# Kernel optimization log

Measured on AMD Instinct MI355X. Metric: run time of the kernel, lower is better.

## Reference

```python
import jax, jax.numpy as jnp
import numpy as np

D_MODEL = 2048
N_HEADS = 16
HEAD_DIM = D_MODEL // N_HEADS  # 128
B, T = 2, 2048


def setup_inputs() -> dict:
    key = jax.random.key(0)
    ks = jax.random.split(key, 9)
    s = 0.02
    x = jax.random.normal(ks[0], (B, T, D_MODEL), dtype=jnp.float32)
    # Per-head projection weights (stacked over heads); torch Linear y = x @ W^T + b,
    # here W is stored as [H, d_model, head_dim] so y = einsum('btc,hcd->bhtd').
    Wq = jax.random.normal(ks[1], (N_HEADS, D_MODEL, HEAD_DIM), dtype=jnp.float32) * s
    bq = jax.random.normal(ks[2], (N_HEADS, HEAD_DIM), dtype=jnp.float32) * s
    Wk = jax.random.normal(ks[3], (N_HEADS, D_MODEL, HEAD_DIM), dtype=jnp.float32) * s
    bk = jax.random.normal(ks[4], (N_HEADS, HEAD_DIM), dtype=jnp.float32) * s
    Wv = jax.random.normal(ks[5], (N_HEADS, D_MODEL, HEAD_DIM), dtype=jnp.float32) * s
    bv = jax.random.normal(ks[6], (N_HEADS, HEAD_DIM), dtype=jnp.float32) * s
    Wo = jax.random.normal(ks[7], (D_MODEL, D_MODEL), dtype=jnp.float32) * s  # used as y @ Wo
    bo = jax.random.normal(ks[8], (D_MODEL,), dtype=jnp.float32) * s
    return {"x": x, "Wq": Wq, "bq": bq, "Wk": Wk, "bk": bk,
            "Wv": Wv, "bv": bv, "Wo": Wo, "bo": bo}


def reference(x, Wq, bq, Wk, bk, Wv, bv, Wo, bo):
    # x: [B, T, C]; per-head Q/K/V projections -> [B, H, T, D]
    Bn, Tn, C = x.shape
    H, _, D = Wq.shape
    scale = D ** (-0.5)
    q = jnp.einsum('btc,hcd->bhtd', x, Wq) + bq[None, :, None, :]
    k = jnp.einsum('btc,hcd->bhtd', x, Wk) + bk[None, :, None, :]
    v = jnp.einsum('btc,hcd->bhtd', x, Wv) + bv[None, :, None, :]
    # scores [B, H, T, T] with additive causal mask (finfo.min above the diagonal)
    scores = jnp.einsum('bhtd,bhsd->bhts', q, k) * scale
    neg = jnp.finfo(scores.dtype).min
    causal = jnp.triu(jnp.full((Tn, Tn), neg, dtype=scores.dtype), k=1)
    probs = jax.nn.softmax(scores + causal, axis=-1)
    y = jnp.einsum('bhts,bhsd->bhtd', probs, v)  # [B, H, T, D]
    # concat heads along feature dim (head order preserved) then output projection
    y = y.transpose(0, 2, 1, 3).reshape(Bn, Tn, H * D)
    return y @ Wo + bo
```

## Files before the change

kernel.cpp:

```cpp
#include <hip/hip_runtime.h>
#include <stdint.h>

typedef unsigned short u16;
typedef __attribute__((ext_vector_type(4))) u16 u16x4;
typedef __attribute__((ext_vector_type(8))) u16 u16x8;
typedef __attribute__((ext_vector_type(8))) __bf16 bf16x8;
typedef __attribute__((ext_vector_type(4))) float f32x4;
typedef __attribute__((ext_vector_type(16))) float f32x16;

#define D_MODEL 2048
#define N_HEADS 16
#define HEAD_DIM 128
#define BATCH 2
#define SEQ 2048
#define M_TOT (BATCH*SEQ)
#define N_QKV (3*D_MODEL)

__device__ __forceinline__ u16 f2b(float f) {
  union { float f; uint32_t u; } c; c.f = f;
  uint32_t u = c.u;
  uint32_t r = (u + 0x7fffu + ((u >> 16) & 1u)) >> 16;
  return (u16)r;
}

__device__ __forceinline__ void gl_lds16(const u16* g, u16* l) {
  __builtin_amdgcn_global_load_lds(
      (const __attribute__((address_space(1))) uint32_t*)g,
      (__attribute__((address_space(3))) uint32_t*)l, 16, 0, 0);
}

template <int N> __device__ __forceinline__ void waitvm() {
  if constexpr (N == 6)      asm volatile("s_waitcnt vmcnt(6)" ::: "memory");
  else if constexpr (N == 5) asm volatile("s_waitcnt vmcnt(5)" ::: "memory");
  else                       asm volatile("s_waitcnt vmcnt(0)" ::: "memory");
}


__global__ void cast_x_kernel(const float* __restrict__ x, u16* __restrict__ xb, int n) {
  int i = (blockIdx.x * blockDim.x + threadIdx.x) * 4;
  if (i >= n) return;
  f32x4 v = *(const f32x4*)(x + i);
  u16x4 o;
  o[0] = f2b(v[0]); o[1] = f2b(v[1]); o[2] = f2b(v[2]); o[3] = f2b(v[3]);
  *(u16x4*)(xb + i) = o;
}

__global__ void trans_wqkv_kernel(const float* __restrict__ Wq, const float* __restrict__ Wk,
                                  const float* __restrict__ Wv, u16* __restrict__ Wt) {
  __shared__ u16 Tl[128][72];
  const int hh = blockIdx.y;
  const int qkv = hh >> 4, h = hh & 15;
  const float* src = (qkv == 0 ? Wq : qkv == 1 ? Wk : Wv) + (size_t)h * 2048 * 128;
  const int k0 = blockIdx.x * 64;
  const int tid = threadIdx.x;
  for (int it = 0; it < 32; ++it) {
    int idx = it * 256 + tid;
    int k = idx >> 7, d = idx & 127;
    Tl[d][k] = f2b(src[(size_t)(k0 + k) * 128 + d]);
  }
  __syncthreads();
  for (int it = 0; it < 32; ++it) {
    int idx = it * 256 + tid;
    int d = idx >> 6, kk = idx & 63;
    Wt[(size_t)(hh * 128 + d) * 2048 + k0 + kk] = Tl[d][kk];
  }
}

__global__ void trans_wo_kernel(const float* __restrict__ Wo, u16* __restrict__ Wot) {
  __shared__ u16 Tl[128][72];
  const int k0 = blockIdx.x * 64;
  const int n0 = blockIdx.y * 128;
  const int tid = threadIdx.x;
  for (int it = 0; it < 32; ++it) {
    int idx = it * 256 + tid;
    int k = idx >> 7, n = idx & 127;
    Tl[n][k] = f2b(Wo[(size_t)(k0 + k) * 2048 + n0 + n]);
  }
  __syncthreads();
  for (int it = 0; it < 32; ++it) {
    int idx = it * 256 + tid;
    int d = idx >> 6, kk = idx & 63;
    Wot[(size_t)(n0 + d) * 2048 + k0 + kk] = Tl[d][kk];
  }
}

__global__ void transpose_v_kernel(const u16* __restrict__ vb, u16* __restrict__ vt) {
  __shared__ u16 Tl[128 * 65];
  const int bh = blockIdx.y;
  const int t0 = blockIdx.x * 64;
  const int tid = threadIdx.x;
  const u16* src = vb + (size_t)bh * 2048 * 128;
  u16* dstp = vt + (size_t)bh * 128 * 2048;
#pragma unroll
  for (int c = 0; c < 4; ++c) {
    int ci = c * 256 + tid;
    int tr = ci >> 4, d0 = (ci & 15) * 8;
    u16x8 v = *(const u16x8*)(src + (size_t)(t0 + tr) * 128 + d0);
#pragma unroll
    for (int e = 0; e < 8; ++e) Tl[(d0 + e) * 65 + tr] = v[e];
  }
  __syncthreads();
#pragma unroll
  for (int it = 0; it < 32; ++it) {
    int idx = it * 256 + tid;
    int d = idx >> 6, tt = idx & 63;
    dstp[(size_t)d * 2048 + t0 + ((tt & 15) * 4 + (tt >> 4))] = Tl[d * 65 + tt];
  }
}

__global__ __launch_bounds__(512, 2) void gemm_qkv_kernel(
    const u16* __restrict__ A, const u16* __restrict__ B,
    u16* __restrict__ qo, u16* __restrict__ ko, u16* __restrict__ vo,
    const float* __restrict__ bq, const float* __restrict__ bk, const float* __restrict__ bv) {
  __shared__ u16 LS[3][20480];
  const int bid0 = blockIdx.x;
  const int gid = (bid0 & 7) * 32 + (bid0 >> 3);
  const int G = gid >> 4, l = gid & 15;
  const int m0 = ((G & 3) * 4 + (l & 3)) * 256;
  const int n0 = ((G >> 2) * 4 + (l >> 2)) * 384;

  const int tid = threadIdx.x, lane = tid & 63, w = tid >> 6;
  const int wm = (w >> 2) * 128, wn = (w & 3) * 96;
  const int l31 = lane & 31, g2 = lane >> 5;

  int aoff[2], boff[3];
#pragma unroll
  for (int l2 = 0; l2 < 2; ++l2) {
    int ci = l2 * 512 + tid, t = ci >> 3, x = (ci & 7) ^ (t & 7);
    aoff[l2] = (m0 + 2 * t + (x >> 2)) * 2048 + (x & 3) * 8;
  }
#pragma unroll
  for (int l2 = 0; l2 < 3; ++l2) {
    int ci = l2 * 512 + tid, t = ci >> 3, x = (ci & 7) ^ (t & 7);
    boff[l2] = (n0 + 2 * t + (x >> 2)) * 2048 + (x & 3) * 8;
  }
  const int adl = tid * 8;
  const int bdl = 8192 + tid * 8;

  f32x16 acc[4][3];
#pragma unroll
  for (int ai = 0; ai < 4; ++ai)
#pragma unroll
    for (int bj = 0; bj < 3; ++bj)
#pragma unroll
      for (int e = 0; e < 16; ++e) acc[ai][bj][e] = 0.f;

#pragma unroll
  for (int t = 0; t < 2; ++t) {
#pragma unroll
    for (int l2 = 0; l2 < 2; ++l2) gl_lds16(A + aoff[l2] + t * 32, LS[t] + adl + l2 * 4096);
#pragma unroll
    for (int l2 = 0; l2 < 3; ++l2) gl_lds16(B + boff[l2] + t * 32, LS[t] + bdl + l2 * 4096);
  }
  waitvm<5>();
  __builtin_amdgcn_s_barrier();

  int s = 0;
  for (int kt = 0; kt < 64; ++kt) {
    if (kt < 62) {
      const int s2 = (s == 0) ? 2 : s - 1;
      const int k2 = (kt + 2) * 32;
#pragma unroll
      for (int l2 = 0; l2 < 2; ++l2) gl_lds16(A + aoff[l2] + k2, LS[s2] + adl + l2 * 4096);
#pragma unroll
      for (int l2 = 0; l2 < 3; ++l2) gl_lds16(B + boff[l2] + k2, LS[s2] + bdl + l2 * 4096);
    }
    const char* base = (const char*)LS[s];
#pragma unroll
    for (int kk = 0; kk < 2; ++kk) {
      bf16x8 af[4];
#pragma unroll
      for (int ai = 0; ai < 4; ++ai) {
        int r = wm + ai * 32 + l31;
        int x = ((r & 1) << 2) | (2 * kk + g2);
        af[ai] = *(const bf16x8*)(base + (r >> 1) * 128 + 16 * (x ^ ((r >> 1) & 7)));
      }
      __builtin_amdgcn_s_setprio(1);
#pragma unroll
      for (int bj = 0; bj < 3; ++bj) {
        int rb = wn + bj * 32 + l31;
        int xb2 = ((rb & 1) << 2) | (2 * kk + g2);
        bf16x8 bfr = *(const bf16x8*)(base + 16384 + (rb >> 1) * 128 + 16 * (xb2 ^ ((rb >> 1) & 7)));
#pragma unroll
        for (int ai = 0; ai < 4; ++ai)
          acc[ai][bj] = __builtin_amdgcn_mfma_f32_32x32x16_bf16(af[ai], bfr, acc[ai][bj], 0, 0, 0);
      }
      __builtin_amdgcn_s_setprio(0);
    }
    if (kt < 62)       waitvm<5>();
    else if (kt == 62) waitvm<0>();
    __builtin_amdgcn_s_barrier();
    s = (s == 2) ? 0 : s + 1;
  }

  const float qscale = 0.08838834764831845f * 1.4426950408889634f;
#pragma unroll
  for (int bj = 0; bj < 3; ++bj) {
    const int n = n0 + wn + bj * 32 + l31;
    const int qkv = n >> 11, hh = (n >> 7) & 15, d = n & 127;
    const float* bias = (qkv == 0) ? bq : (qkv == 1) ? bk : bv;
    u16* dst = (qkv == 0) ? qo : (qkv == 1) ? ko : vo;
    const float bv_ = bias[n & 2047];
#pragma unroll
    for (int ai = 0; ai < 4; ++ai)
#pragma unroll
      for (int e = 0; e < 16; ++e) {
        int row = (e & 3) + 8 * (e >> 2) + 4 * g2;
        int gm = m0 + wm + ai * 32 + row;
        float val = acc[ai][bj][e] + bv_;
        if (qkv == 0) val *= qscale;
        int b = gm >> 11, t = gm & 2047;
        dst[((size_t)(b * 16 + hh) * 2048 + t) * 128 + d] = f2b(val);
      }
  }
}

__global__ __launch_bounds__(512, 2) void gemm_out_kernel(
    const u16* __restrict__ A, const u16* __restrict__ B,
    float* __restrict__ outf, const float* __restrict__ bo) {
  __shared__ u16 LS[3][24576];
  const int bid0 = blockIdx.x;
  const int gid = (bid0 & 7) * 32 + (bid0 >> 3);
  const int G = gid >> 4, l = gid & 15;
  const int m0 = ((G & 3) * 4 + (l & 3)) * 256;
  const int n0 = ((G >> 2) * 4 + (l >> 2)) * 128;

  const int tid = threadIdx.x, lane = tid & 63, w = tid >> 6;
  const int wm = (w >> 1) * 64, wn = (w & 1) * 64;
  const int lr = lane & 15, g = lane >> 4;
  const int kx = (lr & 7) << 4;

  int aoff[4], boff[2];
#pragma unroll
  for (int l2 = 0; l2 < 4; ++l2) {
    int ci = l2 * 512 + tid, r = ci >> 3, gj = ci & 7;
    aoff[l2] = (m0 + r) * 2048 + (gj ^ (r & 7)) * 8;
  }
#pragma unroll
  for (int l2 = 0; l2 < 2; ++l2) {
    int ci = l2 * 512 + tid, r = ci >> 3, gj = ci & 7;
    boff[l2] = (n0 + r) * 2048 + (gj ^ (r & 7)) * 8;
  }
  const int adl = tid * 8;
  const int bdl = 16384 + tid * 8;

  f32x4 acc[4][4];
  const f32x4 zero = {0.f, 0.f, 0.f, 0.f};
#pragma unroll
  for (int ai = 0; ai < 4; ++ai)
#pragma unroll
    for (int bj = 0; bj < 4; ++bj) acc[ai][bj] = zero;

#pragma unroll
  for (int t = 0; t < 2; ++t) {
#pragma unroll
    for (int l2 = 0; l2 < 4; ++l2) gl_lds16(A + aoff[l2] + t * 64, LS[t] + adl + l2 * 4096);
#pragma unroll
    for (int l2 = 0; l2 < 2; ++l2) gl_lds16(B + boff[l2] + t * 64, LS[t] + bdl + l2 * 4096);
  }
  waitvm<6>();
  __builtin_amdgcn_s_barrier();

  int s = 0;
  for (int kt = 0; kt < 32; ++kt) {
    if (kt < 30) {
      const int s2 = (s == 0) ? 2 : s - 1;
      const int k2 = (kt + 2) * 64;
#pragma unroll
      for (int l2 = 0; l2 < 4; ++l2) gl_lds16(A + aoff[l2] + k2, LS[s2] + adl + l2 * 4096);
#pragma unroll
      for (int l2 = 0; l2 < 2; ++l2) gl_lds16(B + boff[l2] + k2, LS[s2] + bdl + l2 * 4096);
    }
    const char* base = (const char*)LS[s];
#pragma unroll
    for (int h = 0; h < 2; ++h) {
      bf16x8 af[4];
#pragma unroll
      for (int ai = 0; ai < 4; ++ai) {
        int r = wm + ai * 16 + lr;
        af[ai] = *(const bf16x8*)(base + r * 128 + ((h * 64 + 16 * g) ^ kx));
      }
      __builtin_amdgcn_s_setprio(1);
#pragma unroll
      for (int bj = 0; bj < 4; ++bj) {
        int rb = wn + bj * 16 + lr;
        bf16x8 bfr = *(const bf16x8*)(base + 32768 + rb * 128 + ((h * 64 + 16 * g) ^ kx));
#pragma unroll
        for (int ai = 0; ai < 4; ++ai)
          acc[ai][bj] = __builtin_amdgcn_mfma_f32_16x16x32_bf16(af[ai], bfr, acc[ai][bj], 0, 0, 0);
      }
      __builtin_amdgcn_s_setprio(0);
    }
    if (kt < 30)       waitvm<6>();
    else if (kt == 30) waitvm<0>();
    __builtin_amdgcn_s_barrier();
    s = (s == 2) ? 0 : s + 1;
  }

  const int rbase = g * 4;
#pragma unroll
  for (int bj = 0; bj < 4; ++bj) {
    const int gn = n0 + wn + bj * 16 + lr;
    const float bv_ = bo[gn];
#pragma unroll
    for (int ai = 0; ai < 4; ++ai)
#pragma unroll
      for (int r = 0; r < 4; ++r) {
        int gm = m0 + wm + ai * 16 + rbase + r;
        outf[(size_t)gm * 2048 + gn] = acc[ai][bj][r] + bv_;
      }
  }
}

__global__ __launch_bounds__(256) void attn_kernel(
    const u16* __restrict__ qg, const u16* __restrict__ kg,
    const u16* __restrict__ vtg, u16* __restrict__ y) {
  __shared__ u16 Kb[2][64 * 128];
  __shared__ u16 Vb[2][128 * 64];
  __shared__ u16 Pl[4][32 * 64];
  const int tid = threadIdx.x, lane = tid & 63, w = tid >> 6;
  const int bid = blockIdx.x;
  const int bh = bid & 31, qt = 15 - (bid >> 5);
  const int b = bh >> 4, h = bh & 15;
  const int lr = lane & 15, lk = (lane >> 4) * 8;
  const u16* Qp = qg + (size_t)bh * (2048 * 128);
  const u16* Kp = kg + (size_t)bh * (2048 * 128);
  const u16* Vp = vtg + (size_t)bh * (128 * 2048);

  int koff[4], voff[4], dstc[4];
#pragma unroll
  for (int c = 0; c < 4; ++c) {
    int ci = c * 256 + tid;
    dstc[c] = ci * 8;
    int kr = ci >> 4, kj = ci & 15;
    koff[c] = kr * 128 + (kj ^ (kr & 7)) * 8;
    int vd = ci >> 3, vj = ci & 7;
    voff[c] = vd * 2048 + (vj ^ (vd & 7)) * 8;
  }
  const int kxor = (lr & 7) << 4;
  const int rbase = (lane >> 4) * 4;
  const f32x4 zero = {0.f, 0.f, 0.f, 0.f};

  const int q0 = qt * 128;
  const int qw = q0 + w * 32;
  const int nt = 2 * qt + 2;

  bf16x8 qf[2][4];
#pragma unroll
  for (int s = 0; s < 2; ++s)
#pragma unroll
    for (int i = 0; i < 4; ++i)
      qf[s][i] = *(const bf16x8*)(Qp + (size_t)(qw + s * 16 + lr) * 128 + i * 32 + lk);

  f32x4 o[2][8];
#pragma unroll
  for (int s = 0; s < 2; ++s)
#pragma unroll
    for (int f = 0; f < 8; ++f) o[s][f] = zero;
  float mrow[2][4], lrow[2][4];
#pragma unroll
  for (int s = 0; s < 2; ++s)
#pragma unroll
    for (int r = 0; r < 4; ++r) { mrow[s][r] = -1e30f; lrow[s][r] = 0.f; }

#pragma unroll
  for (int c = 0; c < 4; ++c) gl_lds16(Kp + koff[c], Kb[0] + dstc[c]);
#pragma unroll
  for (int c = 0; c < 4; ++c) gl_lds16(Vp + voff[c], Vb[0] + dstc[c]);
  __syncthreads();

  int cur = 0;
  for (int t = 0; t < nt; ++t) {
    const int s0 = t * 64;
    if (t + 1 < nt) {
      const size_t skn = (size_t)(s0 + 64) * 128;
#pragma unroll
      for (int c = 0; c < 4; ++c) gl_lds16(Kp + skn + koff[c], Kb[cur ^ 1] + dstc[c]);
#pragma unroll
      for (int c = 0; c < 4; ++c) gl_lds16(Vp + (s0 + 64) + voff[c], Vb[cur ^ 1] + dstc[c]);
    }
    if (s0 <= qw + 31) {
      const char* Kc = (const char*)Kb[cur];
      f32x4 sf[2][4];
      __builtin_amdgcn_s_setprio(1);
#pragma unroll
      for (int sj = 0; sj < 4; ++sj) {
        f32x4 a0 = zero, a1 = zero;
#pragma unroll
        for (int i = 0; i < 4; ++i) {
          bf16x8 kf = *(const bf16x8*)(Kc + ((((sj * 16 + lr) * 256) + (i * 32 + lk) * 2) ^ kxor));
          a0 = __builtin_amdgcn_mfma_f32_16x16x32_bf16(qf[0][i], kf, a0, 0, 0, 0);
          a1 = __builtin_amdgcn_mfma_f32_16x16x32_bf16(qf[1][i], kf, a1, 0, 0, 0);
        }
        sf[0][sj] = a0; sf[1][sj] = a1;
      }
      __builtin_amdgcn_s_setprio(0);

      char* Pc = (char*)Pl[w];
      const bool diag = (s0 + 63 > qw);
      float pmax[2][4];
      bool need = false;
#pragma unroll
      for (int s = 0; s < 2; ++s)
#pragma unroll
        for (int r = 0; r < 4; ++r) {
          if (diag) {
            const int rq = qw + s * 16 + rbase + r;
#pragma unroll
            for (int sj = 0; sj < 4; ++sj)
              if (s0 + sj * 16 + lr > rq) sf[s][sj][r] = -1e30f;
          }
          float pm = fmaxf(fmaxf(sf[s][0][r], sf[s][1][r]),
                           fmaxf(sf[s][2][r], sf[s][3][r]));
          pmax[s][r] = pm;
          need |= (pm > mrow[s][r] + 8.f);
        }
      if (__any(need)) {
#pragma unroll
        for (int s = 0; s < 2; ++s)
#pragma unroll
          for (int r = 0; r < 4; ++r) {
            float pm = pmax[s][r];
            pm = fmaxf(pm, __shfl_xor(pm, 1));
            pm = fmaxf(pm, __shfl_xor(pm, 2));
            pm = fmaxf(pm, __shfl_xor(pm, 4));
            pm = fmaxf(pm, __shfl_xor(pm, 8));
            float mnew = fmaxf(mrow[s][r], pm);
            float sfac = __builtin_amdgcn_exp2f(mrow[s][r] - mnew);
            mrow[s][r] = mnew;
            lrow[s][r] *= sfac;
#pragma unroll
            for (int f = 0; f < 8; ++f) o[s][f][r] *= sfac;
          }
      }
#pragma unroll
      for (int s = 0; s < 2; ++s)
#pragma unroll
        for (int r = 0; r < 4; ++r) {
          const int prow = s * 16 + rbase + r;
          u16x4 pk;
          float ps = 0.f;
#pragma unroll
          for (int sj = 0; sj < 4; ++sj) {
            float p = __builtin_amdgcn_exp2f(sf[s][sj][r] - mrow[s][r]);
            ps += p;
            pk[sj] = f2b(p);
          }
          lrow[s][r] += ps;
          *(u16x4*)(Pc + ((prow * 128 + lr * 8) ^ ((prow & 7) << 4))) = pk;
        }

      const char* Vc = (const char*)Vb[cur];
      __builtin_amdgcn_s_setprio(1);
#pragma unroll
      for (int st = 0; st < 2; ++st) {
        bf16x8 pf0 = *(const bf16x8*)(Pc + (((lr * 128) + (st * 32 + lk) * 2) ^ kxor));
        bf16x8 pf1 = *(const bf16x8*)(Pc + ((((16 + lr) * 128) + (st * 32 + lk) * 2) ^ kxor));
#pragma unroll
        for (int f = 0; f < 8; ++f) {
          bf16x8 vf = *(const bf16x8*)(Vc + ((((f * 16 + lr) * 128) + (st * 32 + lk) * 2) ^ kxor));
          o[0][f] = __builtin_amdgcn_mfma_f32_16x16x32_bf16(pf0, vf, o[0][f], 0, 0, 0);
          o[1][f] = __builtin_amdgcn_mfma_f32_16x16x32_bf16(pf1, vf, o[1][f], 0, 0, 0);
        }
      }
      __builtin_amdgcn_s_setprio(0);
    }
    __syncthreads();
    cur ^= 1;
  }

#pragma unroll
  for (int s = 0; s < 2; ++s)
#pragma unroll
    for (int r = 0; r < 4; ++r) {
      float l = lrow[s][r];
      l += __shfl_xor(l, 1);
      l += __shfl_xor(l, 2);
      l += __shfl_xor(l, 4);
      l += __shfl_xor(l, 8);
      const float rinv = __builtin_amdgcn_rcpf(l);
      const int row = qw + s * 16 + rbase + r;
#pragma unroll
      for (int f = 0; f < 8; ++f)
        y[((size_t)b * 2048 + row) * 2048 + h * 128 + f * 16 + lr] =
            f2b(o[s][f][r] * rinv);
    }
}


extern "C" void kernel_launch(void* const* d_in, const int* in_sizes, int n_in,
                              void* d_out, int out_size, void* d_ws, size_t ws_size,
                              hipStream_t stream) {
  const float* x  = (const float*)d_in[0];
  const float* Wq = (const float*)d_in[1];
  const float* bq = (const float*)d_in[2];
  const float* Wk = (const float*)d_in[3];
  const float* bk = (const float*)d_in[4];
  const float* Wv = (const float*)d_in[5];
  const float* bv = (const float*)d_in[6];
  const float* Wo = (const float*)d_in[7];
  const float* bo = (const float*)d_in[8];
  float* out = (float*)d_out;
  char* ws = (char*)d_ws;

  u16* xb  = (u16*)(ws + 0);
  u16* Wt  = (u16*)(ws + 16777216);
  u16* qb  = (u16*)(ws + 41943040);
  u16* kb  = (u16*)(ws + 58720256);
  u16* vb  = (u16*)(ws + 75497472);
  u16* Wot = Wt;
  u16* vtb = (u16*)(ws + 25165824);
  u16* yb  = xb;

  cast_x_kernel<<<8192, 256, 0, stream>>>(x, xb, M_TOT * D_MODEL);
  trans_wqkv_kernel<<<dim3(32, 48), 256, 0, stream>>>(Wq, Wk, Wv, Wt);
  gemm_qkv_kernel<<<256, 512, 0, stream>>>(xb, Wt, qb, kb, vb, bq, bk, bv);
  trans_wo_kernel<<<dim3(32, 16), 256, 0, stream>>>(Wo, Wot);
  transpose_v_kernel<<<dim3(32, 32), 256, 0, stream>>>(vb, vtb);
  attn_kernel<<<512, 256, 0, stream>>>(qb, kb, vtb, yb);
  gemm_out_kernel<<<256, 512, 0, stream>>>(yb, Wot, out, bo);
}
```

Measured before the change: 282.8 us.

## Fuse prep kernels, write V transposed from QKV GEMM, use packed bf16 convert

Merges the x cast and the QKV weight transpose into one launch. The QKV GEMM epilogue now writes V directly in the permuted transposed layout the attention kernel expects, which removes the separate V transpose kernel and its round trip through memory. The softmax P conversion uses the hardware packed bf16 convert instead of manual rounding. The V epilogue stores are strided along d, so that write pattern may coalesce poorly.

```diff
diff --git a/kernel.cpp b/kernel.cpp
--- a/kernel.cpp
+++ b/kernel.cpp
@@ -35,24 +35,25 @@
   else                       asm volatile("s_waitcnt vmcnt(0)" ::: "memory");
 }
 
-
-__global__ void cast_x_kernel(const float* __restrict__ x, u16* __restrict__ xb, int n) {
-  int i = (blockIdx.x * blockDim.x + threadIdx.x) * 4;
-  if (i >= n) return;
-  f32x4 v = *(const f32x4*)(x + i);
-  u16x4 o;
-  o[0] = f2b(v[0]); o[1] = f2b(v[1]); o[2] = f2b(v[2]); o[3] = f2b(v[3]);
-  *(u16x4*)(xb + i) = o;
-}
-
-__global__ void trans_wqkv_kernel(const float* __restrict__ Wq, const float* __restrict__ Wk,
-                                  const float* __restrict__ Wv, u16* __restrict__ Wt) {
+__global__ __launch_bounds__(256) void prep_kernel(
+    const float* __restrict__ x, u16* __restrict__ xb,
+    const float* __restrict__ Wq, const float* __restrict__ Wk,
+    const float* __restrict__ Wv, u16* __restrict__ Wt) {
   __shared__ u16 Tl[128][72];
-  const int hh = blockIdx.y;
+  const int bid = blockIdx.x, tid = threadIdx.x;
+  if (bid < 8192) {
+    int i = (bid * 256 + tid) * 4;
+    f32x4 v = *(const f32x4*)(x + i);
+    u16x4 o;
+    o[0] = f2b(v[0]); o[1] = f2b(v[1]); o[2] = f2b(v[2]); o[3] = f2b(v[3]);
+    *(u16x4*)(xb + i) = o;
+    return;
+  }
+  const int rel = bid - 8192;
+  const int k0 = (rel & 31) * 64;
+  const int hh = rel >> 5;
   const int qkv = hh >> 4, h = hh & 15;
   const float* src = (qkv == 0 ? Wq : qkv == 1 ? Wk : Wv) + (size_t)h * 2048 * 128;
-  const int k0 = blockIdx.x * 64;
-  const int tid = threadIdx.x;
   for (int it = 0; it < 32; ++it) {
     int idx = it * 256 + tid;
     int k = idx >> 7, d = idx & 127;
@@ -81,30 +82,6 @@
     int idx = it * 256 + tid;
     int d = idx >> 6, kk = idx & 63;
     Wot[(size_t)(n0 + d) * 2048 + k0 + kk] = Tl[d][kk];
-  }
-}
-
-__global__ void transpose_v_kernel(const u16* __restrict__ vb, u16* __restrict__ vt) {
-  __shared__ u16 Tl[128 * 65];
-  const int bh = blockIdx.y;
-  const int t0 = blockIdx.x * 64;
-  const int tid = threadIdx.x;
-  const u16* src = vb + (size_t)bh * 2048 * 128;
-  u16* dstp = vt + (size_t)bh * 128 * 2048;
-#pragma unroll
-  for (int c = 0; c < 4; ++c) {
-    int ci = c * 256 + tid;
-    int tr = ci >> 4, d0 = (ci & 15) * 8;
-    u16x8 v = *(const u16x8*)(src + (size_t)(t0 + tr) * 128 + d0);
-#pragma unroll
-    for (int e = 0; e < 8; ++e) Tl[(d0 + e) * 65 + tr] = v[e];
-  }
-  __syncthreads();
-#pragma unroll
-  for (int it = 0; it < 32; ++it) {
-    int idx = it * 256 + tid;
-    int d = idx >> 6, tt = idx & 63;
-    dstp[(size_t)d * 2048 + t0 + ((tt & 15) * 4 + (tt >> 4))] = Tl[d * 65 + tt];
   }
 }
 
@@ -199,7 +176,7 @@
     const int n = n0 + wn + bj * 32 + l31;
     const int qkv = n >> 11, hh = (n >> 7) & 15, d = n & 127;
     const float* bias = (qkv == 0) ? bq : (qkv == 1) ? bk : bv;
-    u16* dst = (qkv == 0) ? qo : (qkv == 1) ? ko : vo;
+    u16* dst = (qkv == 0) ? qo : ko;
     const float bv_ = bias[n & 2047];
 #pragma unroll
     for (int ai = 0; ai < 4; ++ai)
@@ -210,7 +187,12 @@
         float val = acc[ai][bj][e] + bv_;
         if (qkv == 0) val *= qscale;
         int b = gm >> 11, t = gm & 2047;
-        dst[((size_t)(b * 16 + hh) * 2048 + t) * 128 + d] = f2b(val);
+        if (qkv == 2) {
+          int tt = (t & ~63) | ((t & 15) * 4 + ((t >> 4) & 3));
+          vo[((size_t)(b * 16 + hh)) * 262144 + (size_t)d * 2048 + tt] = f2b(val);
+        } else {
+          dst[((size_t)(b * 16 + hh) * 2048 + t) * 128 + d] = f2b(val);
+        }
       }
   }
 }
@@ -438,16 +420,16 @@
 #pragma unroll
         for (int r = 0; r < 4; ++r) {
           const int prow = s * 16 + rbase + r;
-          u16x4 pk;
-          float ps = 0.f;
-#pragma unroll
-          for (int sj = 0; sj < 4; ++sj) {
-            float p = __builtin_amdgcn_exp2f(sf[s][sj][r] - mrow[s][r]);
-            ps += p;
-            pk[sj] = f2b(p);
-          }
-          lrow[s][r] += ps;
-          *(u16x4*)(Pc + ((prow * 128 + lr * 8) ^ ((prow & 7) << 4))) = pk;
+          float p0 = __builtin_amdgcn_exp2f(sf[s][0][r] - mrow[s][r]);
+          float p1 = __builtin_amdgcn_exp2f(sf[s][1][r] - mrow[s][r]);
+          float p2 = __builtin_amdgcn_exp2f(sf[s][2][r] - mrow[s][r]);
+          float p3 = __builtin_amdgcn_exp2f(sf[s][3][r] - mrow[s][r]);
+          lrow[s][r] += (p0 + p1) + (p2 + p3);
+          uint32_t lo, hi;
+          asm("v_cvt_pk_bf16_f32 %0, %1, %2" : "=v"(lo) : "v"(p0), "v"(p1));
+          asm("v_cvt_pk_bf16_f32 %0, %1, %2" : "=v"(hi) : "v"(p2), "v"(p3));
+          uint32_t* pp = (uint32_t*)(Pc + ((prow * 128 + lr * 8) ^ ((prow & 7) << 4)));
+          pp[0] = lo; pp[1] = hi;
         }
 
       const char* Vc = (const char*)Vb[cur];
@@ -507,16 +489,13 @@
   u16* Wt  = (u16*)(ws + 16777216);
   u16* qb  = (u16*)(ws + 41943040);
   u16* kb  = (u16*)(ws + 58720256);
-  u16* vb  = (u16*)(ws + 75497472);
+  u16* vtb = (u16*)(ws + 75497472);
   u16* Wot = Wt;
-  u16* vtb = (u16*)(ws + 25165824);
   u16* yb  = xb;
 
-  cast_x_kernel<<<8192, 256, 0, stream>>>(x, xb, M_TOT * D_MODEL);
-  trans_wqkv_kernel<<<dim3(32, 48), 256, 0, stream>>>(Wq, Wk, Wv, Wt);
-  gemm_qkv_kernel<<<256, 512, 0, stream>>>(xb, Wt, qb, kb, vb, bq, bk, bv);
+  prep_kernel<<<9728, 256, 0, stream>>>(x, xb, Wq, Wk, Wv, Wt);
+  gemm_qkv_kernel<<<256, 512, 0, stream>>>(xb, Wt, qb, kb, vtb, bq, bk, bv);
   trans_wo_kernel<<<dim3(32, 16), 256, 0, stream>>>(Wo, Wot);
-  transpose_v_kernel<<<dim3(32, 32), 256, 0, stream>>>(vb, vtb);
   attn_kernel<<<512, 256, 0, stream>>>(qb, kb, vtb, yb);
   gemm_out_kernel<<<256, 512, 0, stream>>>(yb, Wot, out, bo);
 }
```

New measurement: 311.3 us. +10.1%, slower.
